# Kernel tuning notes

Measured on AMD Instinct MI355X. Metric: run time of the kernel, lower is better.

## Reference

```python
import jax, jax.numpy as jnp
import numpy as np

B, A = 64, 32            # graphs, atoms per graph
N, E = B * A, B * A * A  # nodes, fully-connected edges (incl. self-loops)
H, LAT = 512, 256        # hidden_dim, latent_dim
L = 4                    # num CSP layers
NF = 10                  # sinusoid frequencies -> dis_dim = 2*NF*3 = 60
MAXA = 100
DIS = 2 * NF * 3
EIN = 2 * H + 9 + DIS    # edge_mlp input width = 1093


def _lin(k, fan_in, shape):
    return jax.random.normal(k, shape, jnp.float32) * (1.0 / np.sqrt(fan_in))


def setup_inputs() -> dict:
    key = jax.random.key(0)
    ks = jax.random.split(key, 20)
    t = jax.random.normal(ks[0], (B, LAT), jnp.float32)
    atom_types = jax.random.randint(ks[1], (N,), 1, MAXA + 1, dtype=jnp.int32)
    frac_coords = jax.random.uniform(ks[2], (N, 3), jnp.float32)
    lattices = jax.random.normal(ks[3], (B, 3, 3), jnp.float32)
    node2graph = jnp.repeat(jnp.arange(B, dtype=jnp.int32), A)
    # fc edges per graph, row-major like dense_to_sparse(block_diag(ones))
    base = (np.arange(B, dtype=np.int64) * A)[:, None]
    ii = np.repeat(np.arange(A), A)
    jj = np.tile(np.arange(A), A)
    src = (base + ii[None, :]).reshape(-1)
    dst = (base + jj[None, :]).reshape(-1)
    edge_index = jnp.asarray(np.stack([src, dst]), dtype=jnp.int32)
    params = dict(
        emb_table=jax.random.normal(ks[4], (MAXA, H), jnp.float32),
        W_latent=_lin(ks[5], H + LAT, (H + LAT, H)), b_latent=jnp.zeros((H,), jnp.float32),
        edge_W1=_lin(ks[6], EIN, (L, EIN, H)), edge_b1=jnp.zeros((L, H), jnp.float32),
        edge_W2=_lin(ks[7], H, (L, H, H)), edge_b2=jnp.zeros((L, H), jnp.float32),
        node_W1=_lin(ks[8], 2 * H, (L, 2 * H, H)), node_b1=jnp.zeros((L, H), jnp.float32),
        node_W2=_lin(ks[9], H, (L, H, H)), node_b2=jnp.zeros((L, H), jnp.float32),
        coord_W=_lin(ks[10], H, (H, 3)),
        lattice_W=_lin(ks[11], H, (H, 9)),
    )
    return dict(t=t, frac_coords=frac_coords, lattices=lattices, **params,
                atom_types=atom_types, node2graph=node2graph, edge_index=edge_index)


def reference(t, frac_coords, lattices, emb_table, W_latent, b_latent,
              edge_W1, edge_b1, edge_W2, edge_b2,
              node_W1, node_b1, node_W2, node_b2,
              coord_W, lattice_W, atom_types, node2graph, edge_index):
    silu = jax.nn.silu
    src, dst = edge_index[0], edge_index[1]
    edge2graph = node2graph[src]
    # gen_edges (fc): frac_diff per edge
    frac_diff = (frac_coords[dst] - frac_coords[src]) % 1.0            # [E,3]
    # SinusoidsEmbedding (same for every layer)
    freqs = 2.0 * jnp.pi * jnp.arange(NF, dtype=jnp.float32)
    fd = (frac_diff[:, :, None] * freqs).reshape(-1, 3 * NF)
    fd_emb = jnp.concatenate([jnp.sin(fd), jnp.cos(fd)], axis=-1)      # [E,60]
    # lattice inner products (ip=True), broadcast to edges
    lat_ip = jnp.einsum('bij,bkj->bik', lattices, lattices).reshape(-1, 9)
    lat_e = lat_ip[edge2graph]                                          # [E,9]
    # node embedding + time conditioning
    nf = emb_table[atom_types - 1]                                      # [N,H]
    nf = jnp.concatenate([nf, t[node2graph]], axis=1) @ W_latent + b_latent
    ones_e = jnp.ones((src.shape[0], 1), nf.dtype)
    for i in range(L):
        hi, hj = nf[src], nf[dst]
        ein = jnp.concatenate([hi, hj, lat_e, fd_emb], axis=1)          # [E,1093]
        ef = silu(silu(ein @ edge_W1[i] + edge_b1[i]) @ edge_W2[i] + edge_b2[i])
        agg = jax.ops.segment_sum(ef, src, num_segments=N)
        deg = jax.ops.segment_sum(ones_e, src, num_segments=N)
        agg = agg / jnp.maximum(deg, 1.0)                               # scatter-mean
        nin = jnp.concatenate([nf, agg], axis=1)                        # [N,2H]
        nf = nf + silu(silu(nin @ node_W1[i] + node_b1[i]) @ node_W2[i] + node_b2[i])
    coord_out = nf @ coord_W                                            # [N,3]
    gf = jax.ops.segment_sum(nf, node2graph, num_segments=B) / A        # graph mean
    lattice_out = (gf @ lattice_W).reshape(-1, 3, 3)
    lattice_out = jnp.einsum('bij,bjk->bik', lattice_out, lattices)     # ip=True
    return (lattice_out, coord_out)
```

## Files before the change

kernel.cpp:

```cpp
#include <hip/hip_runtime.h>
#include <math.h>


typedef short bf16x8 __attribute__((ext_vector_type(8)));
typedef float f32x4 __attribute__((ext_vector_type(4)));

__device__ __forceinline__ float silu_f(float x) {
    float e = __builtin_amdgcn_exp2f(x * -1.44269504088896f);
    return x * __builtin_amdgcn_rcpf(1.0f + e);
}
__device__ __forceinline__ unsigned short f2bf(float x) {
    unsigned int u = __float_as_uint(x);
    u += 0x7fffu + ((u >> 16) & 1u);
    return (unsigned short)(u >> 16);
}
__device__ __forceinline__ unsigned int cvt_pk_bf16(float lo, float hi) {
    unsigned int r;
    asm("v_cvt_pk_bf16_f32 %0, %1, %2" : "=v"(r) : "v"(lo), "v"(hi));
    return r;
}

#define NF_OFF    0
#define UAGG_OFF  (2048*512)
#define VTD_OFF   (2*2048*512)
#define H1_OFF    (VTD_OFF + 64*16384)
#define WBF_OFF   (H1_OFF + 524288)
#define SZ_INITT (512*768)
#define SZ_UVT   (1024*512)
#define SZ_W1DT  (512*64)
#define SZ_W2T   (512*512)
#define SZ_NW1T  (512*1024)
#define SZ_NW2T  (512*512)
#define SZ_LAYER (SZ_UVT+SZ_W1DT+SZ_W2T+SZ_NW1T+SZ_NW2T)
#define WBF_FLOATS ((SZ_INITT + 4*SZ_LAYER + 1)/2)
#define FDP_OFF   (WBF_OFF + WBF_FLOATS)

__global__ __launch_bounds__(256) void k_prep(
    const float* __restrict__ Wl, const float* __restrict__ eW1,
    const float* __restrict__ eW2, const float* __restrict__ nW1,
    const float* __restrict__ nW2, unsigned short* __restrict__ wbf)
{
    __shared__ float tile[32][33];
    int bid = blockIdx.x;
    const float* src; int K; unsigned short* dst; int t;
    if (bid < 384) { src = Wl; K = 768; dst = wbf; t = bid; }
    else {
        int b = bid - 384; int l = b / 1568; int j = b - l * 1568;
        const float* e1 = eW1 + (size_t)l * 1093 * 512;
        unsigned short* base = wbf + SZ_INITT + (size_t)l * SZ_LAYER;
        if (j < 256)      { src = e1;                       K = 512;  dst = base;                                   t = j; }
        else if (j < 512) { src = e1 + 512*512;             K = 512;  dst = base + 512*512;                         t = j-256; }
        else if (j < 544) { src = e1 + 1033*512;            K = 60;   dst = base + SZ_UVT;                          t = j-512; }
        else if (j < 800) { src = eW2 + (size_t)l*512*512;  K = 512;  dst = base + SZ_UVT+SZ_W1DT;                  t = j-544; }
        else if (j <1312) { src = nW1 + (size_t)l*1024*512; K = 1024; dst = base + SZ_UVT+SZ_W1DT+SZ_W2T;           t = j-800; }
        else              { src = nW2 + (size_t)l*512*512;  K = 512;  dst = base + SZ_UVT+SZ_W1DT+SZ_W2T+SZ_NW1T;   t = j-1312; }
    }
    int tr = t >> 4, tc = t & 15;
    int k0 = tr * 32, nn0 = tc * 32;
    {
        int r8 = threadIdx.x >> 5, cc = threadIdx.x & 31;
        #pragma unroll
        for (int rr = 0; rr < 4; ++rr) {
            int row = rr*8 + r8;
            int k = k0 + row;
            tile[row][cc] = (k < K) ? src[(size_t)k*512 + nn0 + cc] : 0.f;
        }
    }
    __syncthreads();
    int nt_loc = threadIdx.x >> 7;
    int l = (threadIdx.x >> 1) & 63;
    int jh = threadIdx.x & 1;
    int lj = l & 15, lh = l >> 4;
    float v0 = tile[lh*8 + jh*4 + 0][nt_loc*16 + lj];
    float v1 = tile[lh*8 + jh*4 + 1][nt_loc*16 + lj];
    float v2 = tile[lh*8 + jh*4 + 2][nt_loc*16 + lj];
    float v3 = tile[lh*8 + jh*4 + 3][nt_loc*16 + lj];
    uint2 pk = { cvt_pk_bf16(v0, v1), cvt_pk_bf16(v2, v3) };
    *(uint2*)&dst[((size_t)(tr*32 + tc*2 + nt_loc)*64 + l)*8 + jh*4] = pk;
}

__global__ __launch_bounds__(64) void k_fd(const float* __restrict__ frac,
                                           unsigned short* __restrict__ fdP)
{
    int bid = blockIdx.x;
    int n0 = bid * 2, g = n0 >> 5;
    int l = threadIdx.x, lj = l & 15, lh = l >> 4;
    float di[2][2][3];
    #pragma unroll
    for (int h = 0; h < 2; ++h)
        #pragma unroll
        for (int dd = 0; dd < 2; ++dd) {
            int dstn = g*32 + dd*16 + lj;
            #pragma unroll
            for (int comp = 0; comp < 3; ++comp) {
                float d = frac[dstn*3 + comp] - frac[(n0+h)*3 + comp];
                d -= floorf(d);
                di[h][dd][comp] = d;
            }
        }
    #pragma unroll
    for (int kt = 0; kt < 2; ++kt)
        #pragma unroll
        for (int mt = 0; mt < 4; ++mt) {
            int h = mt >> 1, dd = mt & 1;
            unsigned int w[4];
            #pragma unroll
            for (int p = 0; p < 4; ++p) {
                float vv[2];
                #pragma unroll
                for (int e = 0; e < 2; ++e) {
                    int k = kt*32 + lh*8 + p*2 + e;
                    float val = 0.f;
                    if (k < 60) {
                        int isCos = k >= 30;
                        int dq = k - (isCos ? 30 : 0);
                        int comp = dq >= 20 ? 2 : (dq >= 10 ? 1 : 0);
                        int f = dq - comp*10;
                        float u = di[h][dd][comp] * (float)f;
                        u -= floorf(u);
                        val = isCos ? __builtin_amdgcn_cosf(u) : __builtin_amdgcn_sinf(u);
                    }
                    vv[e] = val;
                }
                w[p] = cvt_pk_bf16(vv[0], vv[1]);
            }
            uint4 pk = { w[0], w[1], w[2], w[3] };
            *(uint4*)&fdP[(((size_t)bid*8 + kt*4 + mt)*64 + l)*8] = pk;
        }
}

__global__ __launch_bounds__(256) void k_init(
    const float* __restrict__ tvec, const float* __restrict__ emb,
    const unsigned short* __restrict__ WT, const float* __restrict__ bl,
    const int* __restrict__ atom_types, float* __restrict__ nf)
{
    __shared__ __align__(16) unsigned short cat_s[16*768];
    int n0 = (blockIdx.x >> 1) * 16, half = blockIdx.x & 1, tid = threadIdx.x;
    for (int idx = tid; idx < 16*192; idx += 256) {
        int m = idx / 192, q = idx - m * 192;
        int k4 = q * 4, n = n0 + m;
        float4 v;
        if (k4 < 512) v = *(const float4*)&emb[(size_t)(atom_types[n]-1)*512 + k4];
        else          v = *(const float4*)&tvec[(size_t)(n>>5)*256 + (k4-512)];
        uint2 pk = { cvt_pk_bf16(v.x, v.y), cvt_pk_bf16(v.z, v.w) };
        *(uint2*)&cat_s[m*768 + (k4 ^ ((m&7)<<3))] = pk;
    }
    __syncthreads();
    int w = tid >> 6, l = tid & 63, lj = l & 15, lh = l >> 4;
    f32x4 acc[4];
    #pragma unroll
    for (int nt = 0; nt < 4; ++nt) acc[nt] = (f32x4){0.f,0.f,0.f,0.f};
    for (int kt = 0; kt < 24; ++kt) {
        int k = kt*32 + lh*8;
        bf16x8 a = *(const bf16x8*)&cat_s[lj*768 + (k ^ ((lj&7)<<3))];
        #pragma unroll
        for (int nt = 0; nt < 4; ++nt) {
            bf16x8 b = *(const bf16x8*)&WT[(((size_t)kt*32 + half*16 + w*4 + nt)*64 + l)*8];
            acc[nt] = __builtin_amdgcn_mfma_f32_16x16x32_bf16(a, b, acc[nt], 0, 0, 0);
        }
    }
    #pragma unroll
    for (int nt = 0; nt < 4; ++nt) {
        int c = half*256 + w*64 + nt*16 + lj;
        float bv = bl[c];
        #pragma unroll
        for (int r = 0; r < 4; ++r)
            nf[(size_t)(n0 + lh*4 + r)*512 + c] = acc[nt][r] + bv;
    }
}

__global__ __launch_bounds__(256) void k_uv(
    const float* __restrict__ nf, const unsigned short* __restrict__ WT,
    const float* __restrict__ lat, const float* __restrict__ W1c,
    const float* __restrict__ b1, float* __restrict__ Up,
    float* __restrict__ VTD)
{
    __shared__ __align__(16) unsigned short a_s[16*512];
    int n0 = (blockIdx.x >> 1) * 16, half = blockIdx.x & 1;
    int g = n0 >> 5, tid = threadIdx.x;
    for (int idx = tid; idx < 16*128; idx += 256) {
        int m = idx >> 7, q = idx & 127;
        int k4 = q * 4;
        float4 v = *(const float4*)&nf[(size_t)(n0+m)*512 + k4];
        uint2 pk = { cvt_pk_bf16(v.x, v.y), cvt_pk_bf16(v.z, v.w) };
        *(uint2*)&a_s[m*512 + (k4 ^ ((m&7)<<3))] = pk;
    }
    __syncthreads();
    int w = tid >> 6, l = tid & 63, lj = l & 15, lh = l >> 4;
    const unsigned short* Wh = WT + (size_t)half*512*512;
    f32x4 acc[8];
    #pragma unroll
    for (int nt = 0; nt < 8; ++nt) acc[nt] = (f32x4){0.f,0.f,0.f,0.f};
    for (int kt = 0; kt < 16; ++kt) {
        int k = kt*32 + lh*8;
        bf16x8 a = *(const bf16x8*)&a_s[lj*512 + (k ^ ((lj&7)<<3))];
        #pragma unroll
        for (int nt = 0; nt < 8; ++nt) {
            bf16x8 b = *(const bf16x8*)&Wh[(((size_t)kt*32 + w*8 + nt)*64 + l)*8];
            acc[nt] = __builtin_amdgcn_mfma_f32_16x16x32_bf16(a, b, acc[nt], 0, 0, 0);
        }
    }
    if (half == 0) {
        float L[9], lip[9];
        #pragma unroll
        for (int i = 0; i < 9; ++i) L[i] = lat[g*9 + i];
        #pragma unroll
        for (int i = 0; i < 3; ++i)
            #pragma unroll
            for (int kk = 0; kk < 3; ++kk)
                lip[i*3+kk] = L[i*3]*L[kk*3] + L[i*3+1]*L[kk*3+1] + L[i*3+2]*L[kk*3+2];
        #pragma unroll
        for (int nt = 0; nt < 8; ++nt) {
            int c = w*128 + nt*16 + lj;
            float p3 = b1[c];
            #pragma unroll
            for (int t9 = 0; t9 < 9; ++t9) p3 += lip[t9] * W1c[t9*512 + c];
            #pragma unroll
            for (int r = 0; r < 4; ++r)
                Up[(size_t)(n0 + lh*4 + r)*512 + c] = acc[nt][r] + p3;
        }
    } else {
        int dd = (n0 & 31) >> 4;
        #pragma unroll
        for (int nt = 0; nt < 8; ++nt) {
            int ct = w*8 + nt;
            #pragma unroll
            for (int rr = 0; rr < 4; ++rr)
                VTD[(size_t)g*16384 + ct*512 + dd*256 + (lh*4+rr)*16 + lj] = acc[nt][rr];
        }
    }
}

__global__ __launch_bounds__(512) void k_edge(
    const float* __restrict__ Up, const float* __restrict__ VTD,
    const unsigned short* __restrict__ fdP,
    const unsigned short* __restrict__ W1dT,
    const unsigned short* __restrict__ W2T, const float* __restrict__ b2,
    float* __restrict__ agg)
{
    __shared__ __align__(16) unsigned short ef1_s[64*512];
    int n0 = blockIdx.x * 2, g = n0 >> 5, tid = threadIdx.x;
    int wid = tid >> 6, l = tid & 63, lj = l & 15, lh = l >> 4;

    {
        bf16x8 fdf[2][4];
        #pragma unroll
        for (int kt = 0; kt < 2; ++kt)
            #pragma unroll
            for (int mt = 0; mt < 4; ++mt)
                fdf[kt][mt] = *(const bf16x8*)&fdP[(((size_t)blockIdx.x*8 + kt*4 + mt)*64 + l)*8];

        #pragma unroll
        for (int q = 0; q < 4; ++q) {
            int ct = wid*4 + q;
            f32x4 a1[4];
            #pragma unroll
            for (int mt = 0; mt < 4; ++mt)
                a1[mt] = *(const f32x4*)&VTD[(size_t)g*16384 + ct*512 + (mt&1)*256 + lj*16 + lh*4];
            #pragma unroll
            for (int kt = 0; kt < 2; ++kt) {
                bf16x8 wf = *(const bf16x8*)&W1dT[(((size_t)kt*32 + ct)*64 + l)*8];
                #pragma unroll
                for (int mt = 0; mt < 4; ++mt)
                    a1[mt] = __builtin_amdgcn_mfma_f32_16x16x32_bf16(wf, fdf[kt][mt], a1[mt], 0, 0, 0);
            }
            int c0 = wid*64 + q*16 + lh*4;
            float4 bs0 = *(const float4*)&Up[(size_t)n0*512 + c0];
            float4 bs1 = *(const float4*)&Up[(size_t)(n0+1)*512 + c0];
            #pragma unroll
            for (int mt = 0; mt < 4; ++mt) {
                float4 bb = (mt >> 1) ? bs1 : bs0;
                int m = mt*16 + lj;
                float x0 = silu_f(a1[mt][0] + bb.x);
                float x1 = silu_f(a1[mt][1] + bb.y);
                float x2 = silu_f(a1[mt][2] + bb.z);
                float x3 = silu_f(a1[mt][3] + bb.w);
                uint2 pk = { cvt_pk_bf16(x0, x1), cvt_pk_bf16(x2, x3) };
                *(uint2*)&ef1_s[m*512 + (c0 ^ ((m&7)<<3))] = pk;
            }
        }
    }
    __syncthreads();

    f32x4 acc2[4][4];
    #pragma unroll
    for (int mt = 0; mt < 4; ++mt)
        #pragma unroll
        for (int nt = 0; nt < 4; ++nt) acc2[mt][nt] = (f32x4){0.f,0.f,0.f,0.f};

    for (int kt = 0; kt < 16; ++kt) {
        int k = kt*32 + lh*8;
        bf16x8 af[4];
        #pragma unroll
        for (int mt = 0; mt < 4; ++mt) {
            int m = mt*16 + lj;
            af[mt] = *(const bf16x8*)&ef1_s[m*512 + (k ^ ((m&7)<<3))];
        }
        #pragma unroll
        for (int nt = 0; nt < 4; ++nt) {
            bf16x8 bfr = *(const bf16x8*)&W2T[(((size_t)kt*32 + wid*4 + nt)*64 + l)*8];
            #pragma unroll
            for (int mt = 0; mt < 4; ++mt)
                acc2[mt][nt] = __builtin_amdgcn_mfma_f32_16x16x32_bf16(af[mt], bfr, acc2[mt][nt], 0, 0, 0);
        }
    }

    #pragma unroll
    for (int nt = 0; nt < 4; ++nt) {
        int cc = wid*64 + nt*16 + lj;
        float bv = b2[cc];
        float s0 = 0.f, s1 = 0.f;
        #pragma unroll
        for (int mt = 0; mt < 4; ++mt)
            #pragma unroll
            for (int r = 0; r < 4; ++r) {
                float x = silu_f(acc2[mt][nt][r] + bv);
                if (mt < 2) s0 += x; else s1 += x;
            }
        s0 += __shfl_xor(s0, 16); s0 += __shfl_xor(s0, 32);
        s1 += __shfl_xor(s1, 16); s1 += __shfl_xor(s1, 32);
        if (lh == 0) {
            agg[(size_t)n0*512 + cc]     = s0 * (1.0f/32.0f);
            agg[(size_t)(n0+1)*512 + cc] = s1 * (1.0f/32.0f);
        }
    }
}

__global__ __launch_bounds__(256) void k_node1(
    const float* __restrict__ nf, const float* __restrict__ agg,
    const unsigned short* __restrict__ W1T, const float* __restrict__ b1,
    unsigned short* __restrict__ h1g)
{
    __shared__ __align__(16) unsigned short nin_s[16*1024];
    int n0 = (blockIdx.x >> 1) * 16, half = blockIdx.x & 1, tid = threadIdx.x;
    for (int idx = tid; idx < 16*256; idx += 256) {
        int m = idx >> 8, q = idx & 255;
        int k4 = q * 4;
        float4 v = (k4 < 512) ? *(const float4*)&nf[(size_t)(n0+m)*512 + k4]
                              : *(const float4*)&agg[(size_t)(n0+m)*512 + (k4-512)];
        uint2 pk = { cvt_pk_bf16(v.x, v.y), cvt_pk_bf16(v.z, v.w) };
        *(uint2*)&nin_s[m*1024 + (k4 ^ ((m&7)<<3))] = pk;
    }
    __syncthreads();
    int w = tid >> 6, l = tid & 63, lj = l & 15, lh = l >> 4;
    f32x4 acc[4];
    #pragma unroll
    for (int nt = 0; nt < 4; ++nt) acc[nt] = (f32x4){0.f,0.f,0.f,0.f};
    for (int kt = 0; kt < 32; ++kt) {
        int k = kt*32 + lh*8;
        bf16x8 a = *(const bf16x8*)&nin_s[lj*1024 + (k ^ ((lj&7)<<3))];
        #pragma unroll
        for (int nt = 0; nt < 4; ++nt) {
            bf16x8 b = *(const bf16x8*)&W1T[(((size_t)kt*32 + half*16 + w*4 + nt)*64 + l)*8];
            acc[nt] = __builtin_amdgcn_mfma_f32_16x16x32_bf16(a, b, acc[nt], 0, 0, 0);
        }
    }
    #pragma unroll
    for (int nt = 0; nt < 4; ++nt) {
        int c = half*256 + w*64 + nt*16 + lj;
        float bv = b1[c];
        #pragma unroll
        for (int r = 0; r < 4; ++r)
            h1g[(size_t)(n0 + lh*4 + r)*512 + c] = f2bf(silu_f(acc[nt][r] + bv));
    }
}

__global__ __launch_bounds__(256) void k_node2(
    float* __restrict__ nf, const unsigned short* __restrict__ h1g,
    const unsigned short* __restrict__ W2T, const float* __restrict__ b2)
{
    __shared__ __align__(16) unsigned short h1_s[16*512];
    int n0 = (blockIdx.x >> 1) * 16, half = blockIdx.x & 1, tid = threadIdx.x;
    for (int idx = tid; idx < 16*64; idx += 256) {
        int m = idx >> 6, k8 = (idx & 63) * 8;
        bf16x8 v = *(const bf16x8*)&h1g[(size_t)(n0+m)*512 + k8];
        *(bf16x8*)&h1_s[m*512 + (k8 ^ ((m&7)<<3))] = v;
    }
    __syncthreads();
    int w = tid >> 6, l = tid & 63, lj = l & 15, lh = l >> 4;
    f32x4 acc[4];
    #pragma unroll
    for (int nt = 0; nt < 4; ++nt) acc[nt] = (f32x4){0.f,0.f,0.f,0.f};
    for (int kt = 0; kt < 16; ++kt) {
        int k = kt*32 + lh*8;
        bf16x8 a = *(const bf16x8*)&h1_s[lj*512 + (k ^ ((lj&7)<<3))];
        #pragma unroll
        for (int nt = 0; nt < 4; ++nt) {
            bf16x8 b = *(const bf16x8*)&W2T[(((size_t)kt*32 + half*16 + w*4 + nt)*64 + l)*8];
            acc[nt] = __builtin_amdgcn_mfma_f32_16x16x32_bf16(a, b, acc[nt], 0, 0, 0);
        }
    }
    #pragma unroll
    for (int nt = 0; nt < 4; ++nt) {
        int c = half*256 + w*64 + nt*16 + lj;
        float bv = b2[c];
        #pragma unroll
        for (int r = 0; r < 4; ++r) {
            size_t o = (size_t)(n0 + lh*4 + r)*512 + c;
            nf[o] = nf[o] + silu_f(acc[nt][r] + bv);
        }
    }
}

__global__ __launch_bounds__(256) void k_coord(const float* __restrict__ nf,
                                               const float* __restrict__ cW,
                                               float* __restrict__ out) {
    int b = blockIdx.x, t = threadIdx.x;
    int nl = t >> 3, s = t & 7;
    int n = b*32 + nl;
    const float* row = nf + (size_t)n*512 + s*64;
    float p0 = 0.f, p1 = 0.f, p2 = 0.f;
    #pragma unroll
    for (int k4 = 0; k4 < 64; k4 += 4) {
        float4 v = *(const float4*)&row[k4];
        int kg = s*64 + k4;
        p0 += v.x*cW[(kg+0)*3+0] + v.y*cW[(kg+1)*3+0] + v.z*cW[(kg+2)*3+0] + v.w*cW[(kg+3)*3+0];
        p1 += v.x*cW[(kg+0)*3+1] + v.y*cW[(kg+1)*3+1] + v.z*cW[(kg+2)*3+1] + v.w*cW[(kg+3)*3+1];
        p2 += v.x*cW[(kg+0)*3+2] + v.y*cW[(kg+1)*3+2] + v.z*cW[(kg+2)*3+2] + v.w*cW[(kg+3)*3+2];
    }
    p0 += __shfl_xor(p0, 1); p0 += __shfl_xor(p0, 2); p0 += __shfl_xor(p0, 4);
    p1 += __shfl_xor(p1, 1); p1 += __shfl_xor(p1, 2); p1 += __shfl_xor(p1, 4);
    p2 += __shfl_xor(p2, 1); p2 += __shfl_xor(p2, 2); p2 += __shfl_xor(p2, 4);
    if (s == 0) {
        out[576 + n*3 + 0] = p0;
        out[576 + n*3 + 1] = p1;
        out[576 + n*3 + 2] = p2;
    }
}

__global__ __launch_bounds__(256) void k_graph(const float* __restrict__ nf,
                                               const float* __restrict__ lW,
                                               const float* __restrict__ lat,
                                               float* __restrict__ out) {
    __shared__ float gf[512];
    __shared__ float lo9[9];
    int b = blockIdx.x, tid = threadIdx.x;
    float s0 = 0.f, s1 = 0.f;
    for (int r = 0; r < 32; ++r) {
        s0 += nf[(b * 32 + r) * 512 + tid];
        s1 += nf[(b * 32 + r) * 512 + tid + 256];
    }
    gf[tid]       = s0 * (1.f / 32.f);
    gf[tid + 256] = s1 * (1.f / 32.f);
    __syncthreads();
    if (tid < 9) {
        float s = 0.f;
        for (int k = 0; k < 512; ++k) s += gf[k] * lW[k * 9 + tid];
        lo9[tid] = s;
    }
    __syncthreads();
    if (tid < 9) {
        int i = tid / 3, kk = tid - (tid / 3) * 3;
        float s = lo9[i*3+0] * lat[b*9 + 0*3 + kk]
                + lo9[i*3+1] * lat[b*9 + 1*3 + kk]
                + lo9[i*3+2] * lat[b*9 + 2*3 + kk];
        out[b * 9 + tid] = s;
    }
}

extern "C" void kernel_launch(void* const* d_in, const int* in_sizes, int n_in,
                              void* d_out, int out_size, void* d_ws, size_t ws_size,
                              hipStream_t stream)
{
    const float* t    = (const float*)d_in[0];
    const float* frac = (const float*)d_in[1];
    const float* lat  = (const float*)d_in[2];
    const float* emb  = (const float*)d_in[3];
    const float* Wl   = (const float*)d_in[4];
    const float* bl   = (const float*)d_in[5];
    const float* eW1  = (const float*)d_in[6];
    const float* eb1  = (const float*)d_in[7];
    const float* eW2  = (const float*)d_in[8];
    const float* eb2  = (const float*)d_in[9];
    const float* nW1  = (const float*)d_in[10];
    const float* nb1  = (const float*)d_in[11];
    const float* nW2  = (const float*)d_in[12];
    const float* nb2  = (const float*)d_in[13];
    const float* cW   = (const float*)d_in[14];
    const float* lW   = (const float*)d_in[15];
    const int* atom_types = (const int*)d_in[16];

    float* out  = (float*)d_out;
    float* wsf  = (float*)d_ws;
    float* nf   = wsf + NF_OFF;
    float* Uagg = wsf + UAGG_OFF;
    float* VTD  = wsf + VTD_OFF;
    unsigned short* h1g = (unsigned short*)(wsf + H1_OFF);
    unsigned short* wbf = (unsigned short*)(wsf + WBF_OFF);
    unsigned short* fdP = (unsigned short*)(wsf + FDP_OFF);

    k_prep<<<384 + 4*1568, 256, 0, stream>>>(Wl, eW1, eW2, nW1, nW2, wbf);
    k_fd<<<1024, 64, 0, stream>>>(frac, fdP);
    k_init<<<256, 256, 0, stream>>>(t, emb, wbf, bl, atom_types, nf);
    for (int l = 0; l < 4; ++l) {
        const unsigned short* uvT  = wbf + SZ_INITT + (size_t)l * SZ_LAYER;
        const unsigned short* w1dT = uvT + SZ_UVT;
        const unsigned short* w2T  = w1dT + SZ_W1DT;
        const unsigned short* nw1T = w2T + SZ_W2T;
        const unsigned short* nw2T = nw1T + SZ_NW1T;
        k_uv<<<256, 256, 0, stream>>>(nf, uvT, lat,
                                      eW1 + (size_t)l*1093*512 + 1024*512,
                                      eb1 + l*512, Uagg, VTD);
        k_edge<<<1024, 512, 0, stream>>>(Uagg, VTD, fdP, w1dT, w2T,
                                         eb2 + l*512, Uagg);
        k_node1<<<256, 256, 0, stream>>>(nf, Uagg, nw1T, nb1 + l*512, h1g);
        k_node2<<<256, 256, 0, stream>>>(nf, h1g, nw2T, nb2 + l*512);
    }
    k_coord<<<64, 256, 0, stream>>>(nf, cW, out);
    k_graph<<<64, 256, 0, stream>>>(nf, lW, lat, out);
}
```

Baseline: 385.7 us.

## Fuse node MLP and next-layer U/V projection into one kernel

Merges k_node1, k_node2 and the following layer's k_uv into a single k_node kernel. The hidden activation stays in shared memory instead of a global bf16 buffer, and the updated node features are reused in LDS for the next layer's U/V GEMM. This removes two kernel launches per layer and a global round-trip, at the cost of halving the grid to 128 blocks, each doing more serial work, which lowers parallelism. It also adds s_setprio around the MFMA loop in the edge kernel.

```diff
diff --git a/kernel.cpp b/kernel.cpp
--- a/kernel.cpp
+++ b/kernel.cpp
@@ -296,6 +296,7 @@
             int m = mt*16 + lj;
             af[mt] = *(const bf16x8*)&ef1_s[m*512 + (k ^ ((m&7)<<3))];
         }
+        __builtin_amdgcn_s_setprio(1);
         #pragma unroll
         for (int nt = 0; nt < 4; ++nt) {
             bf16x8 bfr = *(const bf16x8*)&W2T[(((size_t)kt*32 + wid*4 + nt)*64 + l)*8];
@@ -303,6 +304,7 @@
             for (int mt = 0; mt < 4; ++mt)
                 acc2[mt][nt] = __builtin_amdgcn_mfma_f32_16x16x32_bf16(af[mt], bfr, acc2[mt][nt], 0, 0, 0);
         }
+        __builtin_amdgcn_s_setprio(0);
     }
 
     #pragma unroll
@@ -326,13 +328,18 @@
     }
 }
 
-__global__ __launch_bounds__(256) void k_node1(
-    const float* __restrict__ nf, const float* __restrict__ agg,
+__global__ __launch_bounds__(256) void k_node(
+    float* __restrict__ nf, const float* __restrict__ agg,
     const unsigned short* __restrict__ W1T, const float* __restrict__ b1,
-    unsigned short* __restrict__ h1g)
+    const unsigned short* __restrict__ W2T, const float* __restrict__ b2,
+    const unsigned short* __restrict__ uvT, const float* __restrict__ lat,
+    const float* __restrict__ W1c, const float* __restrict__ b1e,
+    float* __restrict__ Up, float* __restrict__ VTD, int do_uv)
 {
     __shared__ __align__(16) unsigned short nin_s[16*1024];
-    int n0 = (blockIdx.x >> 1) * 16, half = blockIdx.x & 1, tid = threadIdx.x;
+    __shared__ __align__(16) unsigned short h1_s[16*512];
+    int n0 = blockIdx.x * 16, tid = threadIdx.x;
+    int g = n0 >> 5;
     for (int idx = tid; idx < 16*256; idx += 256) {
         int m = idx >> 8, q = idx & 255;
         int k4 = q * 4;
@@ -343,61 +350,104 @@
     }
     __syncthreads();
     int w = tid >> 6, l = tid & 63, lj = l & 15, lh = l >> 4;
-    f32x4 acc[4];
-    #pragma unroll
-    for (int nt = 0; nt < 4; ++nt) acc[nt] = (f32x4){0.f,0.f,0.f,0.f};
-    for (int kt = 0; kt < 32; ++kt) {
-        int k = kt*32 + lh*8;
-        bf16x8 a = *(const bf16x8*)&nin_s[lj*1024 + (k ^ ((lj&7)<<3))];
-        #pragma unroll
-        for (int nt = 0; nt < 4; ++nt) {
-            bf16x8 b = *(const bf16x8*)&W1T[(((size_t)kt*32 + half*16 + w*4 + nt)*64 + l)*8];
-            acc[nt] = __builtin_amdgcn_mfma_f32_16x16x32_bf16(a, b, acc[nt], 0, 0, 0);
-        }
-    }
-    #pragma unroll
-    for (int nt = 0; nt < 4; ++nt) {
-        int c = half*256 + w*64 + nt*16 + lj;
-        float bv = b1[c];
-        #pragma unroll
-        for (int r = 0; r < 4; ++r)
-            h1g[(size_t)(n0 + lh*4 + r)*512 + c] = f2bf(silu_f(acc[nt][r] + bv));
-    }
-}
-
-__global__ __launch_bounds__(256) void k_node2(
-    float* __restrict__ nf, const unsigned short* __restrict__ h1g,
-    const unsigned short* __restrict__ W2T, const float* __restrict__ b2)
-{
-    __shared__ __align__(16) unsigned short h1_s[16*512];
-    int n0 = (blockIdx.x >> 1) * 16, half = blockIdx.x & 1, tid = threadIdx.x;
-    for (int idx = tid; idx < 16*64; idx += 256) {
-        int m = idx >> 6, k8 = (idx & 63) * 8;
-        bf16x8 v = *(const bf16x8*)&h1g[(size_t)(n0+m)*512 + k8];
-        *(bf16x8*)&h1_s[m*512 + (k8 ^ ((m&7)<<3))] = v;
-    }
-    __syncthreads();
-    int w = tid >> 6, l = tid & 63, lj = l & 15, lh = l >> 4;
-    f32x4 acc[4];
-    #pragma unroll
-    for (int nt = 0; nt < 4; ++nt) acc[nt] = (f32x4){0.f,0.f,0.f,0.f};
+    {
+        f32x4 acc[8];
+        #pragma unroll
+        for (int nt = 0; nt < 8; ++nt) acc[nt] = (f32x4){0.f,0.f,0.f,0.f};
+        for (int kt = 0; kt < 32; ++kt) {
+            int k = kt*32 + lh*8;
+            bf16x8 a = *(const bf16x8*)&nin_s[lj*1024 + (k ^ ((lj&7)<<3))];
+            #pragma unroll
+            for (int nt = 0; nt < 8; ++nt) {
+                bf16x8 b = *(const bf16x8*)&W1T[(((size_t)kt*32 + w*8 + nt)*64 + l)*8];
+                acc[nt] = __builtin_amdgcn_mfma_f32_16x16x32_bf16(a, b, acc[nt], 0, 0, 0);
+            }
+        }
+        #pragma unroll
+        for (int nt = 0; nt < 8; ++nt) {
+            int c = w*128 + nt*16 + lj;
+            float bv = b1[c];
+            #pragma unroll
+            for (int r = 0; r < 4; ++r) {
+                int m = lh*4 + r;
+                h1_s[m*512 + (c ^ ((m&7)<<3))] = f2bf(silu_f(acc[nt][r] + bv));
+            }
+        }
+    }
+    __syncthreads();
+    {
+        f32x4 acc[8];
+        #pragma unroll
+        for (int nt = 0; nt < 8; ++nt) acc[nt] = (f32x4){0.f,0.f,0.f,0.f};
+        for (int kt = 0; kt < 16; ++kt) {
+            int k = kt*32 + lh*8;
+            bf16x8 a = *(const bf16x8*)&h1_s[lj*512 + (k ^ ((lj&7)<<3))];
+            #pragma unroll
+            for (int nt = 0; nt < 8; ++nt) {
+                bf16x8 b = *(const bf16x8*)&W2T[(((size_t)kt*32 + w*8 + nt)*64 + l)*8];
+                acc[nt] = __builtin_amdgcn_mfma_f32_16x16x32_bf16(a, b, acc[nt], 0, 0, 0);
+            }
+        }
+        #pragma unroll
+        for (int nt = 0; nt < 8; ++nt) {
+            int c = w*128 + nt*16 + lj;
+            float bv = b2[c];
+            #pragma unroll
+            for (int r = 0; r < 4; ++r) {
+                int m = lh*4 + r;
+                size_t o = (size_t)(n0 + m)*512 + c;
+                float v = nf[o] + silu_f(acc[nt][r] + bv);
+                nf[o] = v;
+                if (do_uv) nin_s[m*512 + (c ^ ((m&7)<<3))] = f2bf(v);
+            }
+        }
+    }
+    if (!do_uv) return;
+    __syncthreads();
+    f32x4 acc[16];
+    #pragma unroll
+    for (int nt = 0; nt < 16; ++nt) acc[nt] = (f32x4){0.f,0.f,0.f,0.f};
     for (int kt = 0; kt < 16; ++kt) {
         int k = kt*32 + lh*8;
-        bf16x8 a = *(const bf16x8*)&h1_s[lj*512 + (k ^ ((lj&7)<<3))];
-        #pragma unroll
-        for (int nt = 0; nt < 4; ++nt) {
-            bf16x8 b = *(const bf16x8*)&W2T[(((size_t)kt*32 + half*16 + w*4 + nt)*64 + l)*8];
+        bf16x8 a = *(const bf16x8*)&nin_s[lj*512 + (k ^ ((lj&7)<<3))];
+        #pragma unroll
+        for (int nt = 0; nt < 16; ++nt) {
+            int ct = w*16 + nt;
+            const unsigned short* bp = (ct < 32)
+                ? &uvT[(((size_t)kt*32 + ct)*64 + l)*8]
+                : &uvT[512*512 + (((size_t)kt*32 + (ct-32))*64 + l)*8];
+            bf16x8 b = *(const bf16x8*)bp;
             acc[nt] = __builtin_amdgcn_mfma_f32_16x16x32_bf16(a, b, acc[nt], 0, 0, 0);
         }
     }
-    #pragma unroll
-    for (int nt = 0; nt < 4; ++nt) {
-        int c = half*256 + w*64 + nt*16 + lj;
-        float bv = b2[c];
-        #pragma unroll
-        for (int r = 0; r < 4; ++r) {
-            size_t o = (size_t)(n0 + lh*4 + r)*512 + c;
-            nf[o] = nf[o] + silu_f(acc[nt][r] + bv);
+    if (w < 2) {
+        float L[9], lip[9];
+        #pragma unroll
+        for (int i = 0; i < 9; ++i) L[i] = lat[g*9 + i];
+        #pragma unroll
+        for (int i = 0; i < 3; ++i)
+            #pragma unroll
+            for (int kk = 0; kk < 3; ++kk)
+                lip[i*3+kk] = L[i*3]*L[kk*3] + L[i*3+1]*L[kk*3+1] + L[i*3+2]*L[kk*3+2];
+        #pragma unroll
+        for (int nt = 0; nt < 16; ++nt) {
+            int c = w*256 + nt*16 + lj;
+            float p3 = b1e[c];
+            #pragma unroll
+            for (int t9 = 0; t9 < 9; ++t9) p3 += lip[t9] * W1c[t9*512 + c];
+            #pragma unroll
+            for (int r = 0; r < 4; ++r)
+                Up[(size_t)(n0 + lh*4 + r)*512 + c] = acc[nt][r] + p3;
+        }
+    } else {
+        int dd = (n0 & 31) >> 4;
+        #pragma unroll
+        for (int nt = 0; nt < 16; ++nt) {
+            int cc = (w-2)*256 + nt*16 + lj;
+            int ct = cc >> 4;
+            #pragma unroll
+            for (int rr = 0; rr < 4; ++rr)
+                VTD[(size_t)g*16384 + ct*512 + dd*256 + (lh*4+rr)*16 + lj] = acc[nt][rr];
         }
     }
 }
@@ -485,26 +535,33 @@
     float* nf   = wsf + NF_OFF;
     float* Uagg = wsf + UAGG_OFF;
     float* VTD  = wsf + VTD_OFF;
-    unsigned short* h1g = (unsigned short*)(wsf + H1_OFF);
     unsigned short* wbf = (unsigned short*)(wsf + WBF_OFF);
     unsigned short* fdP = (unsigned short*)(wsf + FDP_OFF);
 
     k_prep<<<384 + 4*1568, 256, 0, stream>>>(Wl, eW1, eW2, nW1, nW2, wbf);
     k_fd<<<1024, 64, 0, stream>>>(frac, fdP);
     k_init<<<256, 256, 0, stream>>>(t, emb, wbf, bl, atom_types, nf);
+    {
+        const unsigned short* uvT0 = wbf + SZ_INITT;
+        k_uv<<<256, 256, 0, stream>>>(nf, uvT0, lat,
+                                      eW1 + 1024*512, eb1, Uagg, VTD);
+    }
     for (int l = 0; l < 4; ++l) {
-        const unsigned short* uvT  = wbf + SZ_INITT + (size_t)l * SZ_LAYER;
-        const unsigned short* w1dT = uvT + SZ_UVT;
+        const unsigned short* base = wbf + SZ_INITT + (size_t)l * SZ_LAYER;
+        const unsigned short* w1dT = base + SZ_UVT;
         const unsigned short* w2T  = w1dT + SZ_W1DT;
         const unsigned short* nw1T = w2T + SZ_W2T;
         const unsigned short* nw2T = nw1T + SZ_NW1T;
-        k_uv<<<256, 256, 0, stream>>>(nf, uvT, lat,
-                                      eW1 + (size_t)l*1093*512 + 1024*512,
-                                      eb1 + l*512, Uagg, VTD);
         k_edge<<<1024, 512, 0, stream>>>(Uagg, VTD, fdP, w1dT, w2T,
                                          eb2 + l*512, Uagg);
-        k_node1<<<256, 256, 0, stream>>>(nf, Uagg, nw1T, nb1 + l*512, h1g);
-        k_node2<<<256, 256, 0, stream>>>(nf, h1g, nw2T, nb2 + l*512);
+        int ln = (l < 3) ? l + 1 : l;
+        const unsigned short* uvTn = wbf + SZ_INITT + (size_t)ln * SZ_LAYER;
+        k_node<<<128, 256, 0, stream>>>(nf, Uagg,
+                                        nw1T, nb1 + l*512, nw2T, nb2 + l*512,
+                                        uvTn, lat,
+                                        eW1 + (size_t)ln*1093*512 + 1024*512,
+                                        eb1 + ln*512,
+                                        Uagg, VTD, (l < 3) ? 1 : 0);
     }
     k_coord<<<64, 256, 0, stream>>>(nf, cW, out);
     k_graph<<<64, 256, 0, stream>>>(nf, lW, lat, out);
```

Measured after the change: 624.4 us. +61.9%, slower.
